# Kernel tuning notes

Measured on AMD Instinct MI355X. Metric: run time of the kernel, lower is better.

Reference implementation:

```python
import jax, jax.numpy as jnp
import numpy as np

C = 512          # channels
G = 32           # GroupNorm groups (flax default)
H = 8            # num_heads
EPS = 1e-6       # GroupNorm epsilon (flax default)
SPATIAL = (64, 64)


def setup_inputs() -> dict:
    key = jax.random.key(0)
    k1, k2 = jax.random.split(key)
    x = jax.random.normal(k1, SPATIAL + (C,), dtype=jnp.float32)
    gn_scale = jnp.ones((C,), dtype=jnp.float32)
    gn_bias = jnp.zeros((C,), dtype=jnp.float32)
    w_qkv = jax.random.normal(k2, (C, 3 * C), dtype=jnp.float32) / np.sqrt(C)
    b_qkv = jnp.zeros((3 * C,), dtype=jnp.float32)
    return {"x": x, "gn_scale": gn_scale, "gn_bias": gn_bias,
            "w_qkv": w_qkv, "b_qkv": b_qkv}


def reference(x, gn_scale, gn_bias, w_qkv, b_qkv):
    spatial_shape = x.shape[:-1]
    T = int(np.prod(spatial_shape))
    xf = x.reshape(T, C)

    # GroupNorm over (all spatial positions, channels within group) per group
    xg = xf.reshape(T, G, C // G)
    mean = jnp.mean(xg, axis=(0, 2), keepdims=True)
    var = jnp.var(xg, axis=(0, 2), keepdims=True)
    xn = ((xg - mean) * jax.lax.rsqrt(var + EPS)).reshape(T, C)
    xn = xn * gn_scale + gn_bias

    # QKV projection; note strided split: reshape (T, 3C) -> (T, C, 3)
    qkv = (xn @ w_qkv + b_qkv).reshape(T, C, 3)
    q, k, v = qkv[..., 0], qkv[..., 1], qkv[..., 2]

    ch = C // H
    scale = 1.0 / np.sqrt(np.sqrt(ch))
    qh = (q * scale).reshape(T, H, ch)
    kh = (k * scale).reshape(T, H, ch)
    vh = v.reshape(T, H, ch)

    w = jnp.einsum('thc,shc->ths', qh, kh)      # (T, H, T) attention scores
    w = jax.nn.softmax(w, axis=-1)
    a = jnp.einsum('ths,shc->thc', w, vh)       # (T, H, ch)
    return a.reshape(spatial_shape + (C,))
```

## Files before the change

kernel.cpp:

```cpp
#include <hip/hip_runtime.h>
#include <hip/hip_bf16.h>
#include <stdint.h>

typedef __attribute__((ext_vector_type(8))) short bf16x8;
typedef __attribute__((ext_vector_type(4))) float f32x4;
typedef unsigned short u16;
typedef unsigned int u32;

constexpr int T  = 4096;
constexpr int C  = 512;
constexpr int H  = 8;
constexpr int CH = 64;
constexpr float EPS = 1e-6f;
constexpr float QKS   = 0.35355339059327378f;
constexpr float QKS_Q = 0.35355339059327378f * 1.4426950408889634f;
constexpr float M2    = 11.541560327111707f;

__device__ __forceinline__ float bf2f(u16 u) {
    union { unsigned int i; float f; } v; v.i = ((unsigned int)u) << 16; return v.f;
}
__device__ __forceinline__ u16 f2bf(float f) {
    union { float f; unsigned int i; } v; v.f = f;
    return (u16)((v.i + 0x7FFFu + ((v.i >> 16) & 1u)) >> 16);
}
__device__ __forceinline__ u32 pk2bf(float a, float b) {
    __hip_bfloat162 h = __float22bfloat162_rn(make_float2(a, b));
    u32 r; __builtin_memcpy(&r, &h, 4); return r;
}
__device__ __forceinline__ float ldin(const void* p, int i, int f32) {
    return f32 ? ((const float*)p)[i] : bf2f(((const u16*)p)[i]);
}
__device__ __forceinline__ void async16(const void* g, void* l) {
    __builtin_amdgcn_global_load_lds(
        (const __attribute__((address_space(1))) void*)g,
        (__attribute__((address_space(3))) void*)l,
        16, 0, 0);
}

__global__ void k_stats1(const void* x, float* gs, int* flag) {
    int b = blockIdx.x, tid = threadIdx.x;
    int lane = tid & 63, w = tid >> 6;
    __shared__ int cnt;
    __shared__ float red[4][32][2];
    if (tid == 0) cnt = 0;
    __syncthreads();
    const u16* u = (const u16*)x;
    int huge = 0;
    for (int i = tid; i < 1024; i += 256) {
        float a = fabsf(bf2f(u[i]));
        if (!(a < 1e4f)) huge++;
    }
    if (huge) atomicAdd(&cnt, huge);
    __syncthreads();
    int f32 = (cnt >= 8) ? 1 : 0;
    if (tid == 0) *flag = f32;
    float s1 = 0.f, s2 = 0.f;
    if (f32) {
        const float4* xp = (const float4*)x + b * 4096;
        #pragma unroll
        for (int i = 0; i < 16; i++) {
            float4 v = xp[i * 256 + tid];
            s1 += (v.x + v.y) + (v.z + v.w);
            s2 += (v.x*v.x + v.y*v.y) + (v.z*v.z + v.w*v.w);
        }
        s1 += __shfl_xor(s1, 1); s2 += __shfl_xor(s2, 1);
        s1 += __shfl_xor(s1, 2); s2 += __shfl_xor(s2, 2);
        if ((lane & 3) == 0) {
            int gl = (lane >> 2) + 16 * (w & 1);
            red[w][gl][0] = s1; red[w][gl][1] = s2;
        }
        __syncthreads();
        if (tid < 32) {
            int g = tid, w0 = (g < 16) ? 0 : 1;
            atomicAdd(&gs[g * 2],     red[w0][g][0] + red[w0 + 2][g][0]);
            atomicAdd(&gs[g * 2 + 1], red[w0][g][1] + red[w0 + 2][g][1]);
        }
    } else {
        const uint4* xp = (const uint4*)x + b * 2048;
        #pragma unroll
        for (int i = 0; i < 8; i++) {
            uint4 v = xp[i * 256 + tid];
            float f[8] = { bf2f((u16)(v.x&0xffff)), bf2f((u16)(v.x>>16)),
                           bf2f((u16)(v.y&0xffff)), bf2f((u16)(v.y>>16)),
                           bf2f((u16)(v.z&0xffff)), bf2f((u16)(v.z>>16)),
                           bf2f((u16)(v.w&0xffff)), bf2f((u16)(v.w>>16)) };
            #pragma unroll
            for (int j = 0; j < 8; j++) { s1 += f[j]; s2 += f[j]*f[j]; }
        }
        s1 += __shfl_xor(s1, 1); s2 += __shfl_xor(s2, 1);
        if ((lane & 1) == 0) { red[w][lane >> 1][0] = s1; red[w][lane >> 1][1] = s2; }
        __syncthreads();
        if (tid < 32) {
            int g = tid;
            atomicAdd(&gs[g * 2],     red[0][g][0]+red[1][g][0]+red[2][g][0]+red[3][g][0]);
            atomicAdd(&gs[g * 2 + 1], red[0][g][1]+red[1][g][1]+red[2][g][1]+red[3][g][1]);
        }
    }
}

__global__ void k_fuse(const void* x, const float* __restrict__ gs,
                       const void* gsc, const void* gbi, const void* wq,
                       u16* __restrict__ xn, u16* __restrict__ wt,
                       const int* __restrict__ flag) {
    int bx = blockIdx.x, tid = threadIdx.x;
    int f32 = *flag;
    if (bx < 1024) {
        int idx = (bx * 256 + tid) * 8;
        int c = idx & (C - 1);
        int g = c >> 4;
        float mean = gs[2 * g] * (1.0f / 65536.0f);
        float var  = gs[2 * g + 1] * (1.0f / 65536.0f) - mean * mean;
        float rstd = rsqrtf(var + EPS);
        float v[8];
        if (f32) {
            float4 x0 = *(const float4*)((const float*)x + idx);
            float4 x1 = *(const float4*)((const float*)x + idx + 4);
            v[0]=x0.x; v[1]=x0.y; v[2]=x0.z; v[3]=x0.w;
            v[4]=x1.x; v[5]=x1.y; v[6]=x1.z; v[7]=x1.w;
        } else {
            uint4 u = *(const uint4*)((const u16*)x + idx);
            v[0]=bf2f((u16)(u.x&0xffff)); v[1]=bf2f((u16)(u.x>>16));
            v[2]=bf2f((u16)(u.y&0xffff)); v[3]=bf2f((u16)(u.y>>16));
            v[4]=bf2f((u16)(u.z&0xffff)); v[5]=bf2f((u16)(u.z>>16));
            v[6]=bf2f((u16)(u.w&0xffff)); v[7]=bf2f((u16)(u.w>>16));
        }
        float r[8];
        #pragma unroll
        for (int i = 0; i < 8; i++) {
            float a = rstd * ldin(gsc, c + i, f32);
            r[i] = v[i] * a + (ldin(gbi, c + i, f32) - mean * a);
        }
        uint4 o;
        o.x = pk2bf(r[0], r[1]); o.y = pk2bf(r[2], r[3]);
        o.z = pk2bf(r[4], r[5]); o.w = pk2bf(r[6], r[7]);
        *(uint4*)(xn + idx) = o;
    } else {
        int m = (bx - 1024) * 4 + (tid >> 6);
        int l = tid & 63;
        int k0 = l * 8;
        int col = 3 * (m & 511) + (m >> 9);
        u16 ov[8];
        #pragma unroll
        for (int i = 0; i < 8; i++)
            ov[i] = f2bf(ldin(wq, (k0 + i) * 1536 + col, f32));
        *(uint4*)(wt + m * 512 + k0) = *(uint4*)ov;
    }
}

__global__ __launch_bounds__(256) void k_gemm(
    const u16* __restrict__ xn, const u16* __restrict__ wt,
    const void* __restrict__ bq, const int* __restrict__ flag,
    u16* __restrict__ qh, u16* __restrict__ kh, u16* __restrict__ vt)
{
    __shared__ u16 Al[64 * 64];
    __shared__ u16 Bl[128 * 64];
    __shared__ u16 Tt[4 * 2048];
    int bx = blockIdx.x;
    int bm = bx & 63, bn = bx >> 6;
    int tid = threadIdx.x;
    int w = tid >> 6, lane = tid & 63, quad = lane >> 4, l15 = lane & 15;
    f32x4 acc[4][2] = {};
    const u16* Ag = xn + bm * 64 * 512;
    const u16* Bg = wt + bn * 128 * 512;
    for (int k0 = 0; k0 < 512; k0 += 64) {
        __syncthreads();
        #pragma unroll
        for (int i = 0; i < 2; i++) {
            int L = i * 256 + tid, row = L >> 3, cc = ((L & 7) ^ (row & 7)) * 8;
            async16(Ag + row * 512 + k0 + cc, (void*)(Al + L * 8));
        }
        #pragma unroll
        for (int i = 0; i < 4; i++) {
            int L = i * 256 + tid, row = L >> 3, cc = ((L & 7) ^ (row & 7)) * 8;
            async16(Bg + row * 512 + k0 + cc, (void*)(Bl + L * 8));
        }
        __syncthreads();
        #pragma unroll
        for (int kk = 0; kk < 2; kk++) {
            bf16x8 af[4], bfr[2];
            #pragma unroll
            for (int mi = 0; mi < 4; mi++) {
                int row = mi * 16 + l15;
                af[mi] = *(const bf16x8*)(Al + row * 64 + (((kk * 4 + quad) ^ (row & 7)) * 8));
            }
            #pragma unroll
            for (int ni = 0; ni < 2; ni++) {
                int row = w * 32 + ni * 16 + l15;
                bfr[ni] = *(const bf16x8*)(Bl + row * 64 + (((kk * 4 + quad) ^ (row & 7)) * 8));
            }
            #pragma unroll
            for (int mi = 0; mi < 4; mi++)
                #pragma unroll
                for (int ni = 0; ni < 2; ni++)
                    acc[mi][ni] = __builtin_amdgcn_mfma_f32_16x16x32_bf16(
                        af[mi], bfr[ni], acc[mi][ni], 0, 0, 0);
        }
    }
    int f32 = *flag;
    int t_base = bm * 64;
    int j = bn >> 2;
    if (j < 2) {
        u16* dst = j ? kh : qh;
        float s = j ? QKS : QKS_Q;
        #pragma unroll
        for (int ni = 0; ni < 2; ni++) {
            int n = bn * 128 + w * 32 + ni * 16 + l15;
            int r = n & 511, hh = r >> 6, cc = r & 63;
            float bias = ldin(bq, 3 * r + j, f32);
            #pragma unroll
            for (int mi = 0; mi < 4; mi++) {
                int tq = t_base + mi * 16 + quad * 4;
                #pragma unroll
                for (int rg = 0; rg < 4; rg++)
                    dst[(hh * T + tq + rg) * CH + cc] = f2bf((acc[mi][ni][rg] + bias) * s);
            }
        }
    } else {
        u16* Tw = Tt + w * 2048;
        int rbase = (bn - 8) * 128 + w * 32;
        int hh = rbase >> 6;
        #pragma unroll
        for (int ni = 0; ni < 2; ni++) {
            int r = rbase + ni * 16 + l15;
            float bias = ldin(bq, 3 * (r & 511) + 2, f32);
            int rl = ni * 16 + l15;
            #pragma unroll
            for (int mi = 0; mi < 4; mi++) {
                uint2 pv;
                pv.x = pk2bf(acc[mi][ni][0] + bias, acc[mi][ni][1] + bias);
                pv.y = pk2bf(acc[mi][ni][2] + bias, acc[mi][ni][3] + bias);
                int cs = (mi * 2 + (quad >> 1)) ^ (rl & 7);
                *(uint2*)((u32*)Tw + rl * 32 + cs * 4 + (quad & 1) * 2) = pv;
            }
        }
        int cc_hi = (w & 1) * 32;
        #pragma unroll
        for (int rr = 0; rr < 4; rr++) {
            int rl = rr * 8 + (lane >> 3);
            int g = lane & 7;
            bf16x8 val = *(const bf16x8*)(Tw + rl * 64 + ((g ^ (rl & 7)) * 8));
            *(uint4*)(vt + (hh * CH + cc_hi + rl) * T + t_base + g * 8) = *(uint4*)&val;
        }
    }
}

__global__ __launch_bounds__(256) void k_attn(
    const u16* __restrict__ qh, const u16* __restrict__ kh,
    const u16* __restrict__ vt, float* __restrict__ opart, float* __restrict__ ls)
{
    __shared__ char lds[49152];
    int bx = blockIdx.x;
    int h = bx >> 7, qb = (bx >> 1) & 63, ks = bx & 1;
    int t0 = qb * 64;
    int tid = threadIdx.x;
    int w = tid >> 6, lane = tid & 63, quad = lane >> 4, l15 = lane & 15;
    int p = w >> 1, ww = w & 1;
    int tl = tid & 127;

    u16* Kp = (u16*)(lds + p * 8192);
    u16* Vp = (u16*)(lds + 16384 + p * 8192);
    u16* Pw = (u16*)(lds + 32768 + w * 4096);

    const u16* Kg = kh + (h * T + ks * 2048 + p * 1024) * CH;
    const u16* Vg = vt + h * CH * T + ks * 2048 + p * 1024;

    bf16x8 bq[2][2];
    #pragma unroll
    for (int ni = 0; ni < 2; ni++) {
        int q = ww * 32 + ni * 16 + l15;
        #pragma unroll
        for (int kk = 0; kk < 2; kk++)
            bq[ni][kk] = *(const bf16x8*)(qh + (h * T + t0 + q) * CH + kk * 32 + quad * 8);
    }

    f32x4 o[4][2] = {};
    float lsum[2] = {0.f, 0.f};

    for (int kt = 0; kt < 16; kt++) {
        __syncthreads();
        int s0 = kt * 64;
        #pragma unroll
        for (int i = 0; i < 4; i++) {
            int L = i * 128 + tl;
            int row = L >> 3, cc = ((L & 7) ^ (row & 7)) * 8;
            async16(Kg + (s0 + row) * CH + cc, (void*)(Kp + L * 8));
            async16(Vg + row * T + s0 + cc,    (void*)(Vp + L * 8));
        }
        __syncthreads();
        f32x4 s[4][2] = {};
        #pragma unroll
        for (int kk = 0; kk < 2; kk++)
            #pragma unroll
            for (int mi = 0; mi < 4; mi++) {
                int row = mi * 16 + l15;
                bf16x8 aK = *(const bf16x8*)(Kp + row * 64 + (((kk * 4 + quad) ^ (row & 7)) * 8));
                #pragma unroll
                for (int ni = 0; ni < 2; ni++)
                    s[mi][ni] = __builtin_amdgcn_mfma_f32_16x16x32_bf16(
                        aK, bq[ni][kk], s[mi][ni], 0, 0, 0);
            }
        #pragma unroll
        for (int ni = 0; ni < 2; ni++) {
            int rl = ni * 16 + l15;
            u32* prow = (u32*)Pw + rl * 32;
            float rs = 0.f;
            #pragma unroll
            for (int mi = 0; mi < 4; mi++) {
                float e0 = exp2f(s[mi][ni][0] - M2);
                float e1 = exp2f(s[mi][ni][1] - M2);
                float e2 = exp2f(s[mi][ni][2] - M2);
                float e3 = exp2f(s[mi][ni][3] - M2);
                rs += (e0 + e1) + (e2 + e3);
                int c2 = (mi * 2 + (quad >> 1)) ^ (rl & 7);
                uint2 pv; pv.x = pk2bf(e0, e1); pv.y = pk2bf(e2, e3);
                *(uint2*)(prow + c2 * 4 + (quad & 1) * 2) = pv;
            }
            lsum[ni] += rs;
        }
        #pragma unroll
        for (int kk = 0; kk < 2; kk++) {
            bf16x8 bp[2];
            #pragma unroll
            for (int ni = 0; ni < 2; ni++) {
                int rl = ni * 16 + l15;
                bp[ni] = *(const bf16x8*)(Pw + rl * 64 + (((kk * 4 + quad) ^ (rl & 7)) * 8));
            }
            #pragma unroll
            for (int mi = 0; mi < 4; mi++) {
                int row = mi * 16 + l15;
                bf16x8 av = *(const bf16x8*)(Vp + row * 64 + (((kk * 4 + quad) ^ (row & 7)) * 8));
                #pragma unroll
                for (int ni = 0; ni < 2; ni++)
                    o[mi][ni] = __builtin_amdgcn_mfma_f32_16x16x32_bf16(
                        av, bp[ni], o[mi][ni], 0, 0, 0);
            }
        }
    }
    #pragma unroll
    for (int ni = 0; ni < 2; ni++) {
        lsum[ni] += __shfl_xor(lsum[ni], 16);
        lsum[ni] += __shfl_xor(lsum[ni], 32);
    }
    __syncthreads();
    float* Fp = (float*)(lds + p * 20480);
    float* Lx = (float*)(lds + 40960);
    #pragma unroll
    for (int ni = 0; ni < 2; ni++) {
        int q = ww * 32 + ni * 16 + l15;
        if (quad == 0) Lx[p * 64 + q] = lsum[ni];
        #pragma unroll
        for (int mi = 0; mi < 4; mi++)
            #pragma unroll
            for (int rg = 0; rg < 4; rg++) {
                int d = mi * 16 + quad * 4 + rg;
                Fp[d * 65 + q] = o[mi][ni][rg];
            }
    }
    __syncthreads();
    const float* F0 = (const float*)lds;
    const float* F1 = (const float*)(lds + 20480);
    int q = tid >> 2, dc = (tid & 3) * 16;
    float* od = opart + (((ks * 8 + h) * T) + t0 + q) * 64 + dc;
    #pragma unroll
    for (int i = 0; i < 4; i++) {
        float4 v;
        v.x = F0[(dc+i*4+0)*65+q] + F1[(dc+i*4+0)*65+q];
        v.y = F0[(dc+i*4+1)*65+q] + F1[(dc+i*4+1)*65+q];
        v.z = F0[(dc+i*4+2)*65+q] + F1[(dc+i*4+2)*65+q];
        v.w = F0[(dc+i*4+3)*65+q] + F1[(dc+i*4+3)*65+q];
        *(float4*)(od + i * 4) = v;
    }
    if ((tid & 3) == 0)
        ls[(ks * 8 + h) * T + t0 + q] = Lx[q] + Lx[64 + q];
}

__global__ void k_fin(const float* __restrict__ opart, const float* __restrict__ ls,
                      void* __restrict__ out, const int* __restrict__ flag) {
    int idx = (blockIdx.x * 256 + threadIdx.x) * 8;
    int d0 = idx & 63;
    int ht = idx >> 6;
    int t = ht & (T - 1), h = ht >> 12;
    float inv = 1.0f / (ls[ht] + ls[8 * T + ht]);
    float4 a0 = *(const float4*)(opart + idx);
    float4 a1 = *(const float4*)(opart + idx + 4);
    float4 b0 = *(const float4*)(opart + 2097152 + idx);
    float4 b1 = *(const float4*)(opart + 2097152 + idx + 4);
    float v[8] = { (a0.x+b0.x)*inv, (a0.y+b0.y)*inv, (a0.z+b0.z)*inv, (a0.w+b0.w)*inv,
                   (a1.x+b1.x)*inv, (a1.y+b1.y)*inv, (a1.z+b1.z)*inv, (a1.w+b1.w)*inv };
    int gbase = t * C + h * CH + d0;
    if (*flag) {
        *(float4*)((float*)out + gbase)     = make_float4(v[0], v[1], v[2], v[3]);
        *(float4*)((float*)out + gbase + 4) = make_float4(v[4], v[5], v[6], v[7]);
    } else {
        uint4 o;
        o.x = pk2bf(v[0], v[1]); o.y = pk2bf(v[2], v[3]);
        o.z = pk2bf(v[4], v[5]); o.w = pk2bf(v[6], v[7]);
        *(uint4*)((u16*)out + gbase) = o;
    }
}

extern "C" void kernel_launch(void* const* d_in, const int* in_sizes, int n_in,
                              void* d_out, int out_size, void* d_ws, size_t ws_size,
                              hipStream_t stream) {
    const void* x   = d_in[0];
    const void* gsc = d_in[1];
    const void* gbi = d_in[2];
    const void* wq  = d_in[3];
    const void* bq  = d_in[4];
    char* ws = (char*)d_ws;
    int*   flag = (int*)ws;
    float* gs   = (float*)(ws + 256);
    u16* xn = (u16*)(ws + 8192);
    u16* wt = (u16*)(ws + 4202496);
    u16* qh = (u16*)(ws + 5775360);
    u16* kh = (u16*)(ws + 9969664);
    u16* vt = (u16*)(ws + 14163968);
    float* opart = (float*)(ws + 18358272);
    float* ls    = (float*)(ws + 35135488);

    hipMemsetAsync(gs, 0, 256, stream);
    hipLaunchKernelGGL(k_stats1, dim3(128),  dim3(256), 0, stream, x, gs, flag);
    hipLaunchKernelGGL(k_fuse,   dim3(1408), dim3(256), 0, stream, x, gs, gsc, gbi, wq, xn, wt, flag);
    hipLaunchKernelGGL(k_gemm,   dim3(768),  dim3(256), 0, stream, xn, wt, bq, flag, qh, kh, vt);
    hipLaunchKernelGGL(k_attn,   dim3(1024), dim3(256), 0, stream, qh, kh, vt, opart, ls);
    hipLaunchKernelGGL(k_fin,    dim3(1024), dim3(256), 0, stream, opart, ls, d_out, flag);
}
```

Before: 186.6 us.

## Restructure attention split-K to 4 splits with K double-buffering and tiled weight transpose

The attention kernel moves from a 2-way key split with two intra-block key halves (reduced through LDS) to a 4-way key split where each block handles 128 queries over 1024 keys. K tiles are double-buffered with async loads, V is loaded per iteration, and LDS shrinks so the kernel can use a higher occupancy bound. The weight transpose in k_fuse now goes through shared memory with vectorized row loads instead of strided scalar gathers. k_fin sums four partials, and the workspace is re-laid out so opart aliases xn/wt. The cost is more partial traffic in k_fin and an extra barrier per iteration.

```diff
diff --git a/kernel.cpp b/kernel.cpp
--- a/kernel.cpp
+++ b/kernel.cpp
@@ -135,15 +135,39 @@
         o.z = pk2bf(r[4], r[5]); o.w = pk2bf(r[6], r[7]);
         *(uint4*)(xn + idx) = o;
     } else {
-        int m = (bx - 1024) * 4 + (tid >> 6);
-        int l = tid & 63;
-        int k0 = l * 8;
-        int col = 3 * (m & 511) + (m >> 9);
-        u16 ov[8];
-        #pragma unroll
-        for (int i = 0; i < 8; i++)
-            ov[i] = f2bf(ldin(wq, (k0 + i) * 1536 + col, f32));
-        *(uint4*)(wt + m * 512 + k0) = *(uint4*)ov;
+        __shared__ u16 Wl[48][64];
+        int b = bx - 1024;
+        int k0 = (b >> 5) * 64, c0 = (b & 31) * 48;
+        #pragma unroll
+        for (int it = 0; it < 3; it++) {
+            int u_ = it * 256 + tid;
+            int r = u_ / 12, cu = u_ % 12;
+            int gi = (k0 + r) * 1536 + c0 + cu * 4;
+            float v0, v1, v2, v3;
+            if (f32) {
+                float4 t4 = *(const float4*)((const float*)wq + gi);
+                v0 = t4.x; v1 = t4.y; v2 = t4.z; v3 = t4.w;
+            } else {
+                uint2 t2 = *(const uint2*)((const u16*)wq + gi);
+                v0 = bf2f((u16)(t2.x & 0xffff)); v1 = bf2f((u16)(t2.x >> 16));
+                v2 = bf2f((u16)(t2.y & 0xffff)); v3 = bf2f((u16)(t2.y >> 16));
+            }
+            Wl[cu*4+0][r] = f2bf(v0); Wl[cu*4+1][r] = f2bf(v1);
+            Wl[cu*4+2][r] = f2bf(v2); Wl[cu*4+3][r] = f2bf(v3);
+        }
+        __syncthreads();
+        #pragma unroll
+        for (int it = 0; it < 2; it++) {
+            int u_ = it * 256 + tid;
+            if (u_ < 384) {
+                int mrow = u_ >> 3, kc = u_ & 7;
+                int j = mrow >> 4, cci = mrow & 15;
+                int m = j * 512 + (c0 / 3) + cci;
+                int cl = 3 * cci + j;
+                uint4 val = *(const uint4*)&Wl[cl][kc * 8];
+                *(uint4*)(wt + m * 512 + k0 + kc * 8) = val;
+            }
+        }
     }
 }
 
@@ -244,56 +268,66 @@
     }
 }
 
-__global__ __launch_bounds__(256) void k_attn(
+__global__ __launch_bounds__(256, 4) void k_attn(
     const u16* __restrict__ qh, const u16* __restrict__ kh,
     const u16* __restrict__ vt, float* __restrict__ opart, float* __restrict__ ls)
 {
-    __shared__ char lds[49152];
+    __shared__ char lds[40960];
+    u16* K0 = (u16*)lds;
+    u16* Vl = (u16*)(lds + 16384);
     int bx = blockIdx.x;
-    int h = bx >> 7, qb = (bx >> 1) & 63, ks = bx & 1;
-    int t0 = qb * 64;
+    int h = bx >> 7, qb = (bx >> 2) & 31, ks = bx & 3;
+    int t0 = qb * 128;
     int tid = threadIdx.x;
     int w = tid >> 6, lane = tid & 63, quad = lane >> 4, l15 = lane & 15;
-    int p = w >> 1, ww = w & 1;
-    int tl = tid & 127;
-
-    u16* Kp = (u16*)(lds + p * 8192);
-    u16* Vp = (u16*)(lds + 16384 + p * 8192);
-    u16* Pw = (u16*)(lds + 32768 + w * 4096);
-
-    const u16* Kg = kh + (h * T + ks * 2048 + p * 1024) * CH;
-    const u16* Vg = vt + h * CH * T + ks * 2048 + p * 1024;
+    u16* Pw = (u16*)(lds + 24576 + w * 4096);
+
+    const u16* Kg = kh + (h * T + ks * 1024) * CH;
+    const u16* Vg = vt + h * CH * T + ks * 1024;
 
     bf16x8 bq[2][2];
     #pragma unroll
     for (int ni = 0; ni < 2; ni++) {
-        int q = ww * 32 + ni * 16 + l15;
+        int t = t0 + w * 32 + ni * 16 + l15;
         #pragma unroll
         for (int kk = 0; kk < 2; kk++)
-            bq[ni][kk] = *(const bf16x8*)(qh + (h * T + t0 + q) * CH + kk * 32 + quad * 8);
+            bq[ni][kk] = *(const bf16x8*)(qh + (h * T + t) * CH + kk * 32 + quad * 8);
+    }
+
+    #pragma unroll
+    for (int i = 0; i < 2; i++) {
+        int L = i * 256 + tid, row = L >> 3, cc = ((L & 7) ^ (row & 7)) * 8;
+        async16(Kg + row * CH + cc, (void*)(K0 + L * 8));
     }
 
     f32x4 o[4][2] = {};
     float lsum[2] = {0.f, 0.f};
 
     for (int kt = 0; kt < 16; kt++) {
+        u16* Kc = K0 + (kt & 1) * 4096;
         __syncthreads();
         int s0 = kt * 64;
         #pragma unroll
-        for (int i = 0; i < 4; i++) {
-            int L = i * 128 + tl;
-            int row = L >> 3, cc = ((L & 7) ^ (row & 7)) * 8;
-            async16(Kg + (s0 + row) * CH + cc, (void*)(Kp + L * 8));
-            async16(Vg + row * T + s0 + cc,    (void*)(Vp + L * 8));
-        }
-        __syncthreads();
+        for (int i = 0; i < 2; i++) {
+            int L = i * 256 + tid, row = L >> 3, cc = ((L & 7) ^ (row & 7)) * 8;
+            async16(Vg + row * T + s0 + cc, (void*)(Vl + L * 8));
+        }
+        if (kt < 15) {
+            const u16* Kn = Kg + (s0 + 64) * CH;
+            u16* Kd = K0 + ((kt + 1) & 1) * 4096;
+            #pragma unroll
+            for (int i = 0; i < 2; i++) {
+                int L = i * 256 + tid, row = L >> 3, cc = ((L & 7) ^ (row & 7)) * 8;
+                async16(Kn + row * CH + cc, (void*)(Kd + L * 8));
+            }
+        }
         f32x4 s[4][2] = {};
         #pragma unroll
         for (int kk = 0; kk < 2; kk++)
             #pragma unroll
             for (int mi = 0; mi < 4; mi++) {
-                int row = mi * 16 + l15;
-                bf16x8 aK = *(const bf16x8*)(Kp + row * 64 + (((kk * 4 + quad) ^ (row & 7)) * 8));
+                int r = mi * 16 + l15;
+                bf16x8 aK = *(const bf16x8*)(Kc + r * 64 + (((kk * 4 + quad) ^ (r & 7)) * 8));
                 #pragma unroll
                 for (int ni = 0; ni < 2; ni++)
                     s[mi][ni] = __builtin_amdgcn_mfma_f32_16x16x32_bf16(
@@ -317,6 +351,7 @@
             }
             lsum[ni] += rs;
         }
+        __syncthreads();
         #pragma unroll
         for (int kk = 0; kk < 2; kk++) {
             bf16x8 bp[2];
@@ -327,8 +362,8 @@
             }
             #pragma unroll
             for (int mi = 0; mi < 4; mi++) {
-                int row = mi * 16 + l15;
-                bf16x8 av = *(const bf16x8*)(Vp + row * 64 + (((kk * 4 + quad) ^ (row & 7)) * 8));
+                int r = mi * 16 + l15;
+                bf16x8 av = *(const bf16x8*)(Vl + r * 64 + (((kk * 4 + quad) ^ (r & 7)) * 8));
                 #pragma unroll
                 for (int ni = 0; ni < 2; ni++)
                     o[mi][ni] = __builtin_amdgcn_mfma_f32_16x16x32_bf16(
@@ -342,36 +377,27 @@
         lsum[ni] += __shfl_xor(lsum[ni], 32);
     }
     __syncthreads();
-    float* Fp = (float*)(lds + p * 20480);
-    float* Lx = (float*)(lds + 40960);
+    float* S = (float*)(lds + w * 10240);
     #pragma unroll
     for (int ni = 0; ni < 2; ni++) {
-        int q = ww * 32 + ni * 16 + l15;
-        if (quad == 0) Lx[p * 64 + q] = lsum[ni];
+        int rl = ni * 16 + l15;
+        if (quad == 0) S[2176 + rl] = lsum[ni];
         #pragma unroll
         for (int mi = 0; mi < 4; mi++)
             #pragma unroll
-            for (int rg = 0; rg < 4; rg++) {
-                int d = mi * 16 + quad * 4 + rg;
-                Fp[d * 65 + q] = o[mi][ni][rg];
-            }
-    }
-    __syncthreads();
-    const float* F0 = (const float*)lds;
-    const float* F1 = (const float*)(lds + 20480);
-    int q = tid >> 2, dc = (tid & 3) * 16;
-    float* od = opart + (((ks * 8 + h) * T) + t0 + q) * 64 + dc;
-    #pragma unroll
-    for (int i = 0; i < 4; i++) {
-        float4 v;
-        v.x = F0[(dc+i*4+0)*65+q] + F1[(dc+i*4+0)*65+q];
-        v.y = F0[(dc+i*4+1)*65+q] + F1[(dc+i*4+1)*65+q];
-        v.z = F0[(dc+i*4+2)*65+q] + F1[(dc+i*4+2)*65+q];
-        v.w = F0[(dc+i*4+3)*65+q] + F1[(dc+i*4+3)*65+q];
-        *(float4*)(od + i * 4) = v;
-    }
-    if ((tid & 3) == 0)
-        ls[(ks * 8 + h) * T + t0 + q] = Lx[q] + Lx[64 + q];
+            for (int rg = 0; rg < 4; rg++)
+                S[rl * 68 + mi * 16 + quad * 4 + rg] = o[mi][ni][rg];
+    }
+    int q2 = lane >> 1, dh = (lane & 1) * 32;
+    int t = t0 + w * 32 + q2;
+    float* od = opart + (((ks * 8 + h) * T) + t) * 64 + dh;
+    #pragma unroll
+    for (int i = 0; i < 8; i++)
+        *(f32x4*)(od + i * 4) = *(const f32x4*)(S + q2 * 68 + dh + i * 4);
+    if (lane < 32 && (lane & 1) == 0)
+        ls[(ks * 8 + h) * T + t0 + w * 32 + (lane >> 1)] = S[2176 + (lane >> 1)];
+    if (lane >= 32 && (lane & 1) == 0)
+        ls[(ks * 8 + h) * T + t0 + w * 32 + (lane >> 1)] = S[2176 + (lane >> 1)];
 }
 
 __global__ void k_fin(const float* __restrict__ opart, const float* __restrict__ ls,
@@ -380,13 +406,17 @@
     int d0 = idx & 63;
     int ht = idx >> 6;
     int t = ht & (T - 1), h = ht >> 12;
-    float inv = 1.0f / (ls[ht] + ls[8 * T + ht]);
-    float4 a0 = *(const float4*)(opart + idx);
-    float4 a1 = *(const float4*)(opart + idx + 4);
-    float4 b0 = *(const float4*)(opart + 2097152 + idx);
-    float4 b1 = *(const float4*)(opart + 2097152 + idx + 4);
-    float v[8] = { (a0.x+b0.x)*inv, (a0.y+b0.y)*inv, (a0.z+b0.z)*inv, (a0.w+b0.w)*inv,
-                   (a1.x+b1.x)*inv, (a1.y+b1.y)*inv, (a1.z+b1.z)*inv, (a1.w+b1.w)*inv };
+    float inv = 1.0f / (ls[ht] + ls[32768 + ht] + ls[65536 + ht] + ls[98304 + ht]);
+    float v[8] = {};
+    #pragma unroll
+    for (int ks = 0; ks < 4; ks++) {
+        float4 a0 = *(const float4*)(opart + ks * 2097152 + idx);
+        float4 a1 = *(const float4*)(opart + ks * 2097152 + idx + 4);
+        v[0] += a0.x; v[1] += a0.y; v[2] += a0.z; v[3] += a0.w;
+        v[4] += a1.x; v[5] += a1.y; v[6] += a1.z; v[7] += a1.w;
+    }
+    #pragma unroll
+    for (int i = 0; i < 8; i++) v[i] *= inv;
     int gbase = t * C + h * CH + d0;
     if (*flag) {
         *(float4*)((float*)out + gbase)     = make_float4(v[0], v[1], v[2], v[3]);
@@ -410,17 +440,18 @@
     char* ws = (char*)d_ws;
     int*   flag = (int*)ws;
     float* gs   = (float*)(ws + 256);
-    u16* xn = (u16*)(ws + 8192);
-    u16* wt = (u16*)(ws + 4202496);
-    u16* qh = (u16*)(ws + 5775360);
-    u16* kh = (u16*)(ws + 9969664);
-    u16* vt = (u16*)(ws + 14163968);
-    float* opart = (float*)(ws + 18358272);
-    float* ls    = (float*)(ws + 35135488);
+    char* base = ws + 8192;
+    u16* qh = (u16*)(base);
+    u16* kh = (u16*)(base + 4194304);
+    u16* vt = (u16*)(base + 8388608);
+    u16* xn = (u16*)(base + 12582912);
+    u16* wt = (u16*)(base + 16777216);
+    float* opart = (float*)(base + 12582912);
+    float* ls    = (float*)(base + 46137344);
 
     hipMemsetAsync(gs, 0, 256, stream);
     hipLaunchKernelGGL(k_stats1, dim3(128),  dim3(256), 0, stream, x, gs, flag);
-    hipLaunchKernelGGL(k_fuse,   dim3(1408), dim3(256), 0, stream, x, gs, gsc, gbi, wq, xn, wt, flag);
+    hipLaunchKernelGGL(k_fuse,   dim3(1280), dim3(256), 0, stream, x, gs, gsc, gbi, wq, xn, wt, flag);
     hipLaunchKernelGGL(k_gemm,   dim3(768),  dim3(256), 0, stream, xn, wt, bq, flag, qh, kh, vt);
     hipLaunchKernelGGL(k_attn,   dim3(1024), dim3(256), 0, stream, qh, kh, vt, opart, ls);
     hipLaunchKernelGGL(k_fin,    dim3(1024), dim3(256), 0, stream, opart, ls, d_out, flag);
```

Result: faster. 175.2 us (-6.1%).
